# Performance work log

Hardware: AMD Instinct MI355X
Metric: run time of the kernel (lower is better)

## Reference

```python
import jax, jax.numpy as jnp
import numpy as np

NUM_KEYPOINTS = 2048
SAMPLE_RADIUS = 1.6
NUM_SECTORS = 6
NEG = jnp.float32(-1e10)
POS = jnp.float32(1e10)


def setup_inputs() -> dict:
    key = jax.random.key(0)
    kxy, kz, kc, kcz, kd, ky = jax.random.split(key, 6)
    B, N, M = 2, 65536, 128
    pts_xy = jax.random.uniform(kxy, (B, N, 2), minval=-70.0, maxval=70.0)
    pts_z = jax.random.uniform(kz, (B, N, 1), minval=-3.0, maxval=1.0)
    points = jnp.concatenate([pts_xy, pts_z], axis=-1)  # [B,N,3]
    ctr_xy = jax.random.uniform(kc, (B, M, 2), minval=-60.0, maxval=60.0)
    ctr_z = jax.random.uniform(kcz, (B, M, 1), minval=-2.0, maxval=0.0)
    dims = jax.random.uniform(kd, (B, M, 3), minval=1.0, maxval=4.5)
    yaw = jax.random.uniform(ky, (B, M, 1), minval=-np.pi, maxval=np.pi)
    rois = jnp.concatenate([ctr_xy, ctr_z, dims, yaw], axis=-1)  # [B,M,7]
    return {"points": points, "rois": rois}


def _masked_fps(xyz, mask, K):
    """Farthest point sampling restricted to mask; returns K indices into xyz.
    Matches mmcv furthest_point_sample: squared distances, start at first point."""
    first = jnp.argmax(mask)  # first valid point in original order
    dmin = jnp.where(mask, POS, NEG)

    def step(carry, _):
        dmin, last = carry
        d = jnp.sum((xyz - xyz[last]) ** 2, axis=-1)
        dmin = jnp.minimum(dmin, jnp.where(mask, d, NEG))
        nxt = jnp.argmax(dmin)
        return (dmin, nxt), nxt

    (_, _), rest = jax.lax.scan(step, (dmin, first), None, length=K - 1)
    return jnp.concatenate([first[None], rest])  # [K]


def _spc_single(points, rois):
    """points: [N,3] float, rois: [M,7]. Returns [NUM_KEYPOINTS,3]."""
    N = points.shape[0]
    K = NUM_KEYPOINTS
    # geometric center: z += dz/2 (done in forward before sampling)
    rois = rois.at[:, 2].add(rois[:, 5] * 0.5)
    # --- sample_points_with_roi: point-to-ROI-center distance filter ---
    diff = points[:, None, :] - rois[None, :, 0:3]          # [N,M,3]
    dist = jnp.linalg.norm(diff, axis=-1)                   # [N,M]
    min_dis = jnp.min(dist, axis=-1)
    min_idx = jnp.argmin(dist, axis=-1)
    roi_max_dim = jnp.linalg.norm(rois[min_idx, 3:6] * 0.5, axis=-1)
    valid = min_dis < roi_max_dim + SAMPLE_RADIUS           # [N]
    total = jnp.maximum(jnp.sum(valid), 1)
    # --- sector_fps ---
    sector_size = 2.0 * np.pi / NUM_SECTORS
    angles = jnp.arctan2(points[:, 1], points[:, 0]) + np.pi
    sector = jnp.clip(jnp.floor(angles / sector_size), 0, NUM_SECTORS).astype(jnp.int32)
    masks = valid[None, :] & (sector[None, :] == jnp.arange(NUM_SECTORS)[:, None])  # [S,N]
    cnt = jnp.sum(masks, axis=-1)                           # [S]
    # per-sector budget: min(cnt_k, ceil(cnt_k / total * K)), 0 for empty sectors
    n_k = jnp.minimum(cnt, jnp.ceil(cnt.astype(jnp.float32) * K / total).astype(cnt.dtype))
    fps_idx = jax.vmap(_masked_fps, in_axes=(None, 0, None))(points, masks, K)  # [S,K]
    # concatenate the first n_k picks of each sector in sector order
    offsets = jnp.concatenate([jnp.zeros((1,), n_k.dtype), jnp.cumsum(n_k)[:-1]])
    pos = offsets[:, None] + jnp.arange(K)[None, :]          # [S,K] slot in concat order
    keep = jnp.arange(K)[None, :] < n_k[:, None]
    pos = jnp.where(keep, pos, K)                            # out-of-range -> dropped
    buf = jnp.zeros((K,), jnp.int32)
    buf = buf.at[pos.reshape(-1)].set(fps_idx.reshape(-1).astype(jnp.int32), mode='drop')
    # truncate / cyclic-repeat to exactly K keypoints
    s_total = jnp.maximum(jnp.sum(n_k), 1)
    out_idx = buf[jnp.arange(K) % s_total]
    return points[out_idx]                                   # [K,3]


def reference(points, rois):
    return jax.vmap(_spc_single)(points, rois)  # [B,K,3]
```

## Files before the change

### kernel.cpp

```cpp
#include <hip/hip_runtime.h>
#include <cmath>
#include <cstdint>

#pragma clang fp contract(off)

#define B_ 2
#define N_ 65536
#define M_ 128
#define K_ 2048
#define S_ 6
#define NBLK 256
#define CT 256
#define FPS_T 256
#define NW 4
#define RMAX 16
#define CAP (FPS_T * RMAX)

#define PI_F 3.14159265358979323846f
#define SS_F 1.0471975511965976f

__device__ __forceinline__ unsigned long long wave_max_u64_dpp(unsigned long long key) {
#define DPP_STEP(CTRL)                                                          \
    {                                                                           \
        unsigned lo = (unsigned)key, hi = (unsigned)(key >> 32);                \
        unsigned olo = (unsigned)__builtin_amdgcn_update_dpp(0, (int)lo, CTRL, 0xf, 0xf, true); \
        unsigned ohi = (unsigned)__builtin_amdgcn_update_dpp(0, (int)hi, CTRL, 0xf, 0xf, true); \
        unsigned long long o = ((unsigned long long)ohi << 32) | olo;           \
        if (o > key) key = o;                                                   \
    }
    DPP_STEP(0x111)
    DPP_STEP(0x112)
    DPP_STEP(0x114)
    DPP_STEP(0x118)
    DPP_STEP(0x142)
    DPP_STEP(0x143)
#undef DPP_STEP
    return key;
}

__global__ __launch_bounds__(CT)
void k_classify(const float* __restrict__ points, const float* __restrict__ rois,
                int* __restrict__ sec_id, int* __restrict__ blkcnt) {
    __shared__ float4 sroi[M_];
    __shared__ int lc[8];
    int blk = blockIdx.x;
    int gid = blk * CT + threadIdx.x;
    int b = gid >> 16;
    if (threadIdx.x < M_) {
        const float* r = rois + ((size_t)b * M_ + threadIdx.x) * 7;
        float cz = r[2] + r[5] * 0.5f;
        float hx = r[3] * 0.5f, hy = r[4] * 0.5f, hz = r[5] * 0.5f;
        sroi[threadIdx.x] = make_float4(r[0], r[1], cz, sqrtf((hx*hx + hy*hy) + hz*hz));
    }
    if (threadIdx.x < 8) lc[threadIdx.x] = 0;
    __syncthreads();

    const float* p = points + (size_t)gid * 3;
    float px = p[0], py = p[1], pz = p[2];
    float best = 1e30f; int bi = 0;
    for (int m = 0; m < M_; m++) {
        float4 c = sroi[m];
        float dx = px - c.x, dy = py - c.y, dz = pz - c.z;
        float d = sqrtf((dx*dx + dy*dy) + dz*dz);
        if (d < best) { best = d; bi = m; }
    }
    bool valid = best < (sroi[bi].w + 1.6f);

    float a = atan2f(py, px) + PI_F;
    float fs = floorf(a / SS_F);
    fs = fminf(fmaxf(fs, 0.0f), 6.0f);
    int sec = (int)fs;

    sec_id[gid] = valid ? sec : -1;
    if (valid) atomicAdd(&lc[sec], 1);
    __syncthreads();
    if (threadIdx.x < 8) blkcnt[blk * 8 + threadIdx.x] = lc[threadIdx.x];
}

__global__ void k_plan(const int* __restrict__ blkcnt, int* __restrict__ bbase,
                       int* __restrict__ cnt, int* __restrict__ offv,
                       int* __restrict__ n_needed, int* __restrict__ sec_base,
                       int* __restrict__ s_total) {
    __shared__ int scnt[2][8];
    int t = threadIdx.x;
    if (t < 16) scnt[t >> 3][t & 7] = 0;
    __syncthreads();
    if (t < 14) {
        int b = t / 7, s = t % 7;
        int run = 0;
        for (int j = 0; j < NBLK; j++) {
            int blk = b * NBLK + j;
            int c = blkcnt[blk * 8 + s];
            if (s < 6) bbase[blk * 6 + s] = run;
            run += c;
        }
        scnt[b][s] = run;
        cnt[b * 8 + s] = run;
    }
    __syncthreads();
    if (t < B_) {
        int b = t;
        int total = 0;
        for (int s = 0; s < 7; s++) total += scnt[b][s];
        if (total < 1) total = 1;
        int sb = 0, snk = 0;
        for (int s = 0; s < 6; s++) {
            int cs = scnt[b][s];
            int nk = (int)ceilf((float)cs * 2048.0f / (float)total);
            if (nk > cs) nk = cs;
            offv[b * 6 + s] = snk;
            int need = 0;
            if (snk < K_) { need = K_ - snk; if (need > nk) need = nk; }
            n_needed[b * 6 + s] = need;
            sec_base[b * 6 + s] = sb;
            sb += cs; snk += nk;
        }
        s_total[b] = (snk < 1) ? 1 : snk;
    }
}

__global__ __launch_bounds__(CT)
void k_compact(const float* __restrict__ points, const int* __restrict__ sec_id,
               const int* __restrict__ sec_base, const int* __restrict__ bbase,
               int* __restrict__ comp_idx, float4* __restrict__ comp_xyz) {
    __shared__ int lc[4 * 6];
    __shared__ int sbase[6], blkb[6];
    int blk = blockIdx.x;
    int b = blk >> 8;
    int tid = threadIdx.x, lane = tid & 63, wid = tid >> 6;
    if (tid < 6) sbase[tid] = sec_base[b * 6 + tid];
    else if (tid >= 64 && tid < 70) blkb[tid - 64] = bbase[blk * 6 + (tid - 64)];
    int gid = blk * CT + tid;
    int sec = sec_id[gid];
    unsigned long long mymask = 0;
    for (int s = 0; s < 6; s++) {
        unsigned long long m = __ballot(sec == s);
        if (sec == s) mymask = m;
        if (lane == 0) lc[wid * 6 + s] = __popcll(m);
    }
    __syncthreads();
    if (sec >= 0 && sec < 6) {
        int woff = 0;
        for (int w = 0; w < wid; w++) woff += lc[w * 6 + sec];
        int rank = __popcll(mymask & ((1ull << lane) - 1ull));
        int addr = b * N_ + sbase[sec] + blkb[sec] + woff + rank;
        const float* p = points + (size_t)gid * 3;
        comp_idx[addr] = gid & (N_ - 1);
        comp_xyz[addr] = make_float4(p[0], p[1], p[2], 0.0f);
    }
}

__global__ __launch_bounds__(FPS_T, 3)
void k_fps(const int* __restrict__ cnt, const int* __restrict__ sec_base,
           const int* __restrict__ offv, const int* __restrict__ n_needed,
           const float4* __restrict__ comp_xyz,
           float* __restrict__ dmin_g, int* __restrict__ buf) {
    __shared__ float4 sxyz[CAP];
    __shared__ int pick_lds[K_];
    __shared__ unsigned long long skey[2][NW];
    int b = blockIdx.x / S_, s = blockIdx.x % S_;
    int need = n_needed[b * 6 + s];
    if (need <= 0) return;
    int cs = cnt[b * 8 + s];
    int base = b * N_ + sec_base[b * 6 + s];
    const float4* cxyz = comp_xyz + base;
    int off = b * K_ + offv[b * 6 + s];
    int tid = threadIdx.x, lane = tid & 63, wid = tid >> 6;

    if (cs <= CAP) {
        float px[RMAX], py[RMAX], pz[RMAX], dmv[RMAX];
        #pragma unroll
        for (int r = 0; r < RMAX; r++) {
            if (r * FPS_T < cs) {
                int i = tid + r * FPS_T;
                if (i < cs) {
                    float4 q = cxyz[i];
                    sxyz[i] = q;
                    px[r] = q.x; py[r] = q.y; pz[r] = q.z;
                    dmv[r] = 1e10f;
                }
            }
        }
        if (tid == 0) pick_lds[0] = 0;
        __syncthreads();
        float4 l4 = sxyz[0];
        float lx = l4.x, ly = l4.y, lz = l4.z;

        #pragma unroll 1
        for (int k = 1; k < need; k++) {
            unsigned long long key = 0;
            #pragma unroll
            for (int r = 0; r < RMAX; r++) {
                if (r * FPS_T < cs) {
                    int i = tid + r * FPS_T;
                    if (i < cs) {
                        float dx = px[r] - lx, dy = py[r] - ly, dz = pz[r] - lz;
                        float d = (dx*dx + dy*dy) + dz*dz;
                        float nd = fminf(dmv[r], d);
                        dmv[r] = nd;
                        unsigned long long kk =
                            ((unsigned long long)__float_as_uint(nd) << 32) | (unsigned)(~(unsigned)i);
                        if (kk > key) key = kk;
                    }
                }
            }
            key = wave_max_u64_dpp(key);
            int par = k & 1;
            if (lane == 63) skey[par][wid] = key;
            __syncthreads();
            unsigned long long bk = skey[par][0];
            if (skey[par][1] > bk) bk = skey[par][1];
            if (skey[par][2] > bk) bk = skey[par][2];
            if (skey[par][3] > bk) bk = skey[par][3];
            int bix = (int)(~(unsigned)(bk & 0xFFFFFFFFull));
            if (tid == 0) pick_lds[k] = bix;
            float4 n4 = sxyz[bix];
            lx = n4.x; ly = n4.y; lz = n4.z;
        }
        __syncthreads();
        #pragma unroll 1
        for (int i = tid; i < need; i += FPS_T)
            buf[off + i] = base + pick_lds[i];
    } else {
        float* dm = dmin_g + base;
        if (tid == 0) pick_lds[0] = 0;
        __syncthreads();
        float4 f0 = cxyz[0];
        float lx = f0.x, ly = f0.y, lz = f0.z;
        #pragma unroll 1
        for (int k = 1; k < need; k++) {
            unsigned long long key = 0;
            #pragma unroll 1
            for (int i = tid; i < cs; i += FPS_T) {
                float4 q = cxyz[i];
                float dx = q.x - lx, dy = q.y - ly, dz = q.z - lz;
                float d = (dx*dx + dy*dy) + dz*dz;
                float prev = (k == 1) ? 1e10f : dm[i];
                float nd = fminf(prev, d);
                dm[i] = nd;
                unsigned long long kk =
                    ((unsigned long long)__float_as_uint(nd) << 32) | (unsigned)(~(unsigned)i);
                if (kk > key) key = kk;
            }
            key = wave_max_u64_dpp(key);
            int par = k & 1;
            if (lane == 63) skey[par][wid] = key;
            __syncthreads();
            unsigned long long bk = skey[par][0];
            if (skey[par][1] > bk) bk = skey[par][1];
            if (skey[par][2] > bk) bk = skey[par][2];
            if (skey[par][3] > bk) bk = skey[par][3];
            int bix = (int)(~(unsigned)(bk & 0xFFFFFFFFull));
            if (tid == 0) pick_lds[k] = bix;
            float4 n4 = cxyz[bix];
            lx = n4.x; ly = n4.y; lz = n4.z;
        }
        __syncthreads();
        #pragma unroll 1
        for (int i = tid; i < need; i += FPS_T)
            buf[off + i] = base + pick_lds[i];
    }
}

__global__ void k_out(const float* __restrict__ points, const int* __restrict__ buf,
                      const int* __restrict__ comp_idx, const int* __restrict__ s_total,
                      float* __restrict__ out) {
    int i = blockIdx.x * 256 + threadIdx.x;
    if (i >= B_ * K_) return;
    int b = i / K_, j = i % K_;
    int st = s_total[b];
    int g = buf[b * K_ + (j % st)];
    int idx = comp_idx[g];
    const float* p = points + ((size_t)b * N_ + idx) * 3;
    float* o = out + (size_t)i * 3;
    o[0] = p[0]; o[1] = p[1]; o[2] = p[2];
}

extern "C" void kernel_launch(void* const* d_in, const int* in_sizes, int n_in,
                              void* d_out, int out_size, void* d_ws, size_t ws_size,
                              hipStream_t stream) {
    const float* points = (const float*)d_in[0];
    const float* rois   = (const float*)d_in[1];
    float* out = (float*)d_out;

    char* w = (char*)d_ws;
    auto carve = [&](size_t bytes) -> char* {
        char* p = w; w += (bytes + 255) & ~(size_t)255; return p;
    };
    int*    sec_id   = (int*)   carve((size_t)B_ * N_ * sizeof(int));
    int*    blkcnt   = (int*)   carve((size_t)B_ * NBLK * 8 * sizeof(int));
    int*    bbase    = (int*)   carve((size_t)B_ * NBLK * 6 * sizeof(int));
    int*    cnt      = (int*)   carve((size_t)B_ * 8 * sizeof(int));
    int*    offv     = (int*)   carve((size_t)B_ * 6 * sizeof(int));
    int*    n_needed = (int*)   carve((size_t)B_ * 6 * sizeof(int));
    int*    sec_base = (int*)   carve((size_t)B_ * 6 * sizeof(int));
    int*    s_total  = (int*)   carve((size_t)B_ * sizeof(int));
    int*    buf      = (int*)   carve((size_t)B_ * K_ * sizeof(int));
    int*    comp_idx = (int*)   carve((size_t)B_ * N_ * sizeof(int));
    float4* comp_xyz = (float4*)carve((size_t)B_ * N_ * sizeof(float4));
    float*  dmin_g   = (float*) carve((size_t)B_ * N_ * sizeof(float));

    hipLaunchKernelGGL(k_classify, dim3(B_ * NBLK), dim3(CT), 0, stream,
                       points, rois, sec_id, blkcnt);
    hipLaunchKernelGGL(k_plan, dim3(1), dim3(64), 0, stream,
                       blkcnt, bbase, cnt, offv, n_needed, sec_base, s_total);
    hipLaunchKernelGGL(k_compact, dim3(B_ * NBLK), dim3(CT), 0, stream,
                       points, sec_id, sec_base, bbase, comp_idx, comp_xyz);
    hipLaunchKernelGGL(k_fps, dim3(B_ * S_), dim3(FPS_T), 0, stream,
                       cnt, sec_base, offv, n_needed, comp_xyz, dmin_g, buf);
    hipLaunchKernelGGL(k_out, dim3((B_ * K_ + 255) / 256), dim3(256), 0, stream,
                       points, buf, comp_idx, s_total, out);
}
```

Baseline: 471.7 us.

## Double FPS block width to 512 threads and tree-reduce argmax keys

Raises the FPS block from 256 to 512 threads (8 waves) and halves the per-thread register slice from 16 to 8 points, keeping the same LDS capacity. The per-thread max is split into four independent accumulators to shorten the dependency chain, and the cross-wave reduction becomes a tree over 8 wave keys. This spreads each sector's distance updates over more lanes to cut per-iteration latency, at the cost of a larger barrier, one extra reduction level and a lower occupancy hint. It also adds an unroll pragma to the serial count loop in the planning kernel.

```diff
diff --git a/kernel.cpp b/kernel.cpp
--- a/kernel.cpp
+++ b/kernel.cpp
@@ -11,9 +11,9 @@
 #define S_ 6
 #define NBLK 256
 #define CT 256
-#define FPS_T 256
-#define NW 4
-#define RMAX 16
+#define FPS_T 512
+#define NW 8
+#define RMAX 8
 #define CAP (FPS_T * RMAX)
 
 #define PI_F 3.14159265358979323846f
@@ -88,6 +88,7 @@
     if (t < 14) {
         int b = t / 7, s = t % 7;
         int run = 0;
+        #pragma unroll 16
         for (int j = 0; j < NBLK; j++) {
             int blk = b * NBLK + j;
             int c = blkcnt[blk * 8 + s];
@@ -150,7 +151,7 @@
     }
 }
 
-__global__ __launch_bounds__(FPS_T, 3)
+__global__ __launch_bounds__(FPS_T, 2)
 void k_fps(const int* __restrict__ cnt, const int* __restrict__ sec_base,
            const int* __restrict__ offv, const int* __restrict__ n_needed,
            const float4* __restrict__ comp_xyz,
@@ -188,7 +189,7 @@
 
         #pragma unroll 1
         for (int k = 1; k < need; k++) {
-            unsigned long long key = 0;
+            unsigned long long t[4] = {0ull, 0ull, 0ull, 0ull};
             #pragma unroll
             for (int r = 0; r < RMAX; r++) {
                 if (r * FPS_T < cs) {
@@ -200,18 +201,28 @@
                         dmv[r] = nd;
                         unsigned long long kk =
                             ((unsigned long long)__float_as_uint(nd) << 32) | (unsigned)(~(unsigned)i);
-                        if (kk > key) key = kk;
+                        if (kk > t[r & 3]) t[r & 3] = kk;
                     }
                 }
             }
+            unsigned long long ta = (t[1] > t[0]) ? t[1] : t[0];
+            unsigned long long tb = (t[3] > t[2]) ? t[3] : t[2];
+            unsigned long long key = (tb > ta) ? tb : ta;
             key = wave_max_u64_dpp(key);
             int par = k & 1;
             if (lane == 63) skey[par][wid] = key;
             __syncthreads();
-            unsigned long long bk = skey[par][0];
-            if (skey[par][1] > bk) bk = skey[par][1];
-            if (skey[par][2] > bk) bk = skey[par][2];
-            if (skey[par][3] > bk) bk = skey[par][3];
+            unsigned long long q0 = skey[par][0], q1 = skey[par][1];
+            unsigned long long q2 = skey[par][2], q3 = skey[par][3];
+            unsigned long long q4 = skey[par][4], q5 = skey[par][5];
+            unsigned long long q6 = skey[par][6], q7 = skey[par][7];
+            q0 = (q1 > q0) ? q1 : q0;
+            q2 = (q3 > q2) ? q3 : q2;
+            q4 = (q5 > q4) ? q5 : q4;
+            q6 = (q7 > q6) ? q7 : q6;
+            q0 = (q2 > q0) ? q2 : q0;
+            q4 = (q6 > q4) ? q6 : q4;
+            unsigned long long bk = (q4 > q0) ? q4 : q0;
             int bix = (int)(~(unsigned)(bk & 0xFFFFFFFFull));
             if (tid == 0) pick_lds[k] = bix;
             float4 n4 = sxyz[bix];
@@ -246,10 +257,17 @@
             int par = k & 1;
             if (lane == 63) skey[par][wid] = key;
             __syncthreads();
-            unsigned long long bk = skey[par][0];
-            if (skey[par][1] > bk) bk = skey[par][1];
-            if (skey[par][2] > bk) bk = skey[par][2];
-            if (skey[par][3] > bk) bk = skey[par][3];
+            unsigned long long q0 = skey[par][0], q1 = skey[par][1];
+            unsigned long long q2 = skey[par][2], q3 = skey[par][3];
+            unsigned long long q4 = skey[par][4], q5 = skey[par][5];
+            unsigned long long q6 = skey[par][6], q7 = skey[par][7];
+            q0 = (q1 > q0) ? q1 : q0;
+            q2 = (q3 > q2) ? q3 : q2;
+            q4 = (q5 > q4) ? q5 : q4;
+            q6 = (q7 > q6) ? q7 : q6;
+            q0 = (q2 > q0) ? q2 : q0;
+            q4 = (q6 > q4) ? q6 : q4;
+            unsigned long long bk = (q4 > q0) ? q4 : q0;
             int bix = (int)(~(unsigned)(bk & 0xFFFFFFFFull));
             if (tid == 0) pick_lds[k] = bix;
             float4 n4 = cxyz[bix];
```

Result: faster. 436.2 us (-7.5%).
